# Performance work log

Measured on AMD Instinct MI355X. Metric: run time of the kernel, lower is better.

Reference implementation:

```python
import jax, jax.numpy as jnp
import numpy as np

B, N, H = 8, 2000, 64  # batch, num_nodes(=input_dim), hidden(num_gru_units)


def _laplacian_self_loop(a):
    # batched: norm = D^{-1/2} (A + I) D^{-1/2}
    m = a + jnp.eye(a.shape[-1], dtype=a.dtype)
    d_inv_sqrt = jnp.sum(m, axis=-1) ** -0.5  # (B, N)
    return d_inv_sqrt[..., :, None] * m * d_inv_sqrt[..., None, :]


def _graph_conv(inputs, hidden_flat, adj, windd, W2, b2, W3, b3, W, b, out_dim):
    b_, _, n = inputs.shape
    # dynamic wind-based adjacency
    wind_now = inputs[:, 2, :] * 360.0  # (B, N)
    direction = jnp.abs(windd[None, :, :] - wind_now[:, :, None])  # (B, N, N)
    direction = jnp.where(direction > 360.0, 180.0, direction)
    d1 = jnp.maximum(jnp.cos(direction * (jnp.pi / 180.0)), 0.0)
    a = d1 @ W2.T + b2 + (adj @ W3.T + b3)[None]  # (B, N, N)
    a1 = _laplacian_self_loop(jnp.maximum(a, 0.0))
    # graph conv: concat [x, h] then A @ [.] then Linear
    x = jnp.concatenate([inputs[:, 0, :, None], hidden_flat.reshape(b_, n, H)], axis=2)  # (B,N,H+1)
    y = jnp.einsum('bij,bjh->bih', a1, x) @ W.T + b  # (B, N, out_dim)
    return y.reshape(b_, n * out_dim)


def reference(inputs, hidden_state, adj, windd, W2, b2, W3, b3, W1a, b1a, W1b, b1b, Wca1, Wca2, Wsa):
    b_, _, n = inputs.shape
    conc = _graph_conv(inputs, hidden_state, adj, windd, W2, b2, W3, b3, W1a, b1a, 2 * H)
    conc = conc.reshape(b_, 2 * H, n)  # faithful reshape (input_dim == N)
    # --- channel attention (CBAM) ---
    avg = jnp.mean(conc, axis=2, keepdims=True)  # (B, 2H, 1)
    mx = jnp.max(conc, axis=2, keepdims=True)
    def fc(v):
        return jnp.einsum('oc,bcx->box', Wca2, jax.nn.relu(jnp.einsum('oc,bcx->box', Wca1, v)))
    ca = jax.nn.sigmoid(fc(avg) + fc(mx))  # (B, 2H, 1)
    conc = ca * conc
    # --- spatial attention ---
    s = jnp.stack([jnp.mean(conc, axis=1), jnp.max(conc, axis=1)], axis=1)  # (B, 2, N)
    sa = jax.lax.conv_general_dilated(s, Wsa, window_strides=(1,), padding=((3, 3),),
                                      dimension_numbers=('NCH', 'OIH', 'NCH'))  # (B,1,N)
    conc = jax.nn.sigmoid(sa) * conc
    # --- GRU gates ---
    conc = jax.nn.sigmoid(conc.reshape(b_, 2 * H * n))
    r, u = jnp.split(conc, 2, axis=1)  # each (B, N*H)
    c = jnp.tanh(_graph_conv(inputs, r * hidden_state, adj, windd, W2, b2, W3, b3, W1b, b1b, H))
    new_hidden_state = u * hidden_state + (1.0 - u) * c
    return new_hidden_state


def setup_inputs() -> dict:
    key = jax.random.key(0)
    ks = jax.random.split(key, 12)
    inputs = jax.random.uniform(ks[0], (B, 3, N), dtype=jnp.float32)
    hidden_state = jax.random.normal(ks[1], (B, N * H), dtype=jnp.float32) * 0.1
    adj = jax.random.uniform(ks[2], (N, N), dtype=jnp.float32)
    windd = jax.random.uniform(ks[3], (N, N), dtype=jnp.float32) * 360.0
    sN = 1.0 / np.sqrt(N)
    W2 = jax.random.normal(ks[4], (N, N), dtype=jnp.float32) * sN
    b2 = jnp.zeros((N,), jnp.float32)
    W3 = jax.random.normal(ks[5], (N, N), dtype=jnp.float32) * sN
    b3 = jnp.zeros((N,), jnp.float32)
    sI = 1.0 / np.sqrt(H + 1)
    W1a = jax.random.normal(ks[6], (2 * H, H + 1), dtype=jnp.float32) * sI
    b1a = jnp.ones((2 * H,), jnp.float32)  # bias=1.0 in graph_conv1
    W1b = jax.random.normal(ks[7], (H, H + 1), dtype=jnp.float32) * sI
    b1b = jnp.zeros((H,), jnp.float32)
    Wca1 = jax.random.normal(ks[8], (2 * H // 16, 2 * H), dtype=jnp.float32) * (1.0 / np.sqrt(2 * H))
    Wca2 = jax.random.normal(ks[9], (2 * H, 2 * H // 16), dtype=jnp.float32) * (1.0 / np.sqrt(2 * H // 16))
    Wsa = jax.random.normal(ks[10], (1, 2, 7), dtype=jnp.float32) * (1.0 / np.sqrt(14))
    return {'inputs': inputs, 'hidden_state': hidden_state, 'adj': adj, 'windd': windd,
            'W2': W2, 'b2': b2, 'W3': W3, 'b3': b3, 'W1a': W1a, 'b1a': b1a,
            'W1b': W1b, 'b1b': b1b, 'Wca1': Wca1, 'Wca2': Wca2, 'Wsa': Wsa}
```

## Files before the change

### kernel.cpp

```cpp
#include <hip/hip_runtime.h>

#define NN 2000
#define BB 8
#define P  2048

typedef __attribute__((ext_vector_type(8))) short bf16x8;
typedef __attribute__((ext_vector_type(4))) float f32x4;

__device__ __forceinline__ float sigf(float x) { return 1.0f / (1.0f + expf(-x)); }

__device__ __forceinline__ short f2bf(float x) {
    union { float f; unsigned u; } v; v.f = x;
    unsigned r = v.u + 0x7fffu + ((v.u >> 16) & 1u);
    return (short)(r >> 16);
}
__device__ __forceinline__ float bf2f(short h) {
    union { unsigned u; float f; } v; v.u = ((unsigned)(unsigned short)h) << 16; return v.f;
}

__device__ __forceinline__ void gl2lds16(const short* g, short* l) {
    __builtin_amdgcn_global_load_lds(
        (const __attribute__((address_space(1))) void*)g,
        (__attribute__((address_space(3))) void*)l, 16, 0, 0);
}

__global__ __launch_bounds__(256) void k_cvtW(
    const float* __restrict__ s0, const float* __restrict__ s1, const float* __restrict__ s2,
    short* __restrict__ d0, short* __restrict__ d1, short* __restrict__ d2)
{
    const int i = blockIdx.x, sel = blockIdx.y, t = threadIdx.x;
    const float* s = (sel == 0) ? s0 : (sel == 1) ? s1 : s2;
    short* d = ((sel == 0) ? d0 : (sel == 1) ? d1 : d2) + ((size_t)i) * P + t * 8;
    bf16x8 v;
#pragma unroll
    for (int e = 0; e < 8; ++e) v[e] = 0;
    if (i < NN && t < 250) {
        const float* p = s + (size_t)i * NN + t * 8;
        float4 x0 = *(const float4*)p;
        float4 x1 = *(const float4*)(p + 4);
        float a[8] = {x0.x,x0.y,x0.z,x0.w,x1.x,x1.y,x1.z,x1.w};
#pragma unroll
        for (int e = 0; e < 8; ++e) v[e] = f2bf(a[e]);
    }
    *(bf16x8*)d = v;
}

__global__ __launch_bounds__(256) void k_cvtD1(
    const float* __restrict__ windd, const float* __restrict__ inputs, short* __restrict__ d1bf)
{
    const int i = blockIdx.x, t = threadIdx.x;
    const bool live = (i < NN) && (t < 250);
    float a[8];
    if (live) {
        const float* p = windd + (size_t)i * NN + t * 8;
        float4 x0 = *(const float4*)p;
        float4 x1 = *(const float4*)(p + 4);
        a[0]=x0.x; a[1]=x0.y; a[2]=x0.z; a[3]=x0.w;
        a[4]=x1.x; a[5]=x1.y; a[6]=x1.z; a[7]=x1.w;
    }
#pragma unroll
    for (int b = 0; b < BB; ++b) {
        bf16x8 v;
#pragma unroll
        for (int e = 0; e < 8; ++e) v[e] = 0;
        if (live) {
            const float wn = inputs[(size_t)b * 3 * NN + 2 * NN + i] * 360.0f;
#pragma unroll
            for (int e = 0; e < 8; ++e) {
                float dd = fabsf(a[e] - wn);
                dd = (dd > 360.0f) ? 180.0f : dd;
                float c = __cosf(dd * 0.01745329251994329577f);
                v[e] = f2bf(fmaxf(c, 0.0f));
            }
        }
        *(bf16x8*)(d1bf + ((size_t)b * P + i) * P + t * 8) = v;
    }
}

template<int EPI, int OUTD>
__global__ __launch_bounds__(256) void k_mfma(
    const short* __restrict__ Abase, const short* __restrict__ Bbase,
    const float* __restrict__ bias, const short* __restrict__ adjw,
    void* __restrict__ Cout, float* __restrict__ part, size_t aBatch)
{
    __shared__ short shA[4096];
    __shared__ short shB[4096];
    const int t = threadIdx.x;
    const int w = t >> 6, lane = t & 63;
    const int wr = w >> 1, wc = w & 1;

    int i0, j0, b, kt = 0;
    if (EPI == 1) {
        const int id = blockIdx.x;
        const int lg = (id & 7) * 256 + (id >> 3);
        b = lg >> 8;
        const int rem = lg & 255;
        i0 = (rem >> 4) * 128;
        j0 = (rem & 15) * 128;
    } else if (EPI == 2) {
        i0 = blockIdx.x * 128; j0 = 0; kt = blockIdx.y; b = blockIdx.z;
    } else {
        i0 = blockIdx.x * 128; j0 = blockIdx.y * 128; b = 0;
    }
    const int kb = (EPI == 2) ? kt * (P / 4) : 0;
    const int ke = (EPI == 2) ? kt * (P / 4) + (P / 4) : P;

    const short* A  = Abase + (size_t)b * aBatch;
    const short* Bm = Bbase + ((EPI == 2) ? (size_t)b * 128 * P : (size_t)0);

    f32x4 acc[4][4];
#pragma unroll
    for (int m = 0; m < 4; ++m)
#pragma unroll
        for (int n = 0; n < 4; ++n) acc[m][n] = (f32x4){0.f, 0.f, 0.f, 0.f};

    const int lidx0 = w * 128 + lane;
    const int lidx1 = lidx0 + 64;
    const short* aS0 = A  + (size_t)(i0 + (lidx0 >> 2)) * P + (lidx0 & 3) * 8;
    const short* aS1 = A  + (size_t)(i0 + (lidx1 >> 2)) * P + (lidx1 & 3) * 8;
    const short* bS0 = Bm + (size_t)(j0 + (lidx0 >> 2)) * P + (lidx0 & 3) * 8;
    const short* bS1 = Bm + (size_t)(j0 + (lidx1 >> 2)) * P + (lidx1 & 3) * 8;
    short* ldA0 = shA + (w * 128) * 8;
    short* ldA1 = shA + (w * 128 + 64) * 8;
    short* ldB0 = shB + (w * 128) * 8;
    short* ldB1 = shB + (w * 128 + 64) * 8;

    const int lr = lane & 15, lq = lane >> 4;
    const int aoff = (wr * 64 + lr) * 32 + lq * 8;
    const int boff = (wc * 64 + lr) * 32 + lq * 8;

    for (int k0 = kb; k0 < ke; k0 += 32) {
        gl2lds16(aS0 + k0, ldA0);
        gl2lds16(aS1 + k0, ldA1);
        gl2lds16(bS0 + k0, ldB0);
        gl2lds16(bS1 + k0, ldB1);
        __syncthreads();
        bf16x8 aF[4], bF[4];
#pragma unroll
        for (int m = 0; m < 4; ++m) aF[m] = *(const bf16x8*)(shA + aoff + m * 512);
#pragma unroll
        for (int n = 0; n < 4; ++n) bF[n] = *(const bf16x8*)(shB + boff + n * 512);
#pragma unroll
        for (int m = 0; m < 4; ++m)
#pragma unroll
            for (int n = 0; n < 4; ++n)
                acc[m][n] = __builtin_amdgcn_mfma_f32_16x16x32_bf16(aF[m], bF[n], acc[m][n], 0, 0, 0);
        __syncthreads();
    }

    const int rbase = i0 + wr * 64 + lq * 4;
    const int cbase = j0 + wc * 64 + lr;
#pragma unroll
    for (int m = 0; m < 4; ++m) {
#pragma unroll
        for (int n = 0; n < 4; ++n) {
            const int col = cbase + n * 16;
#pragma unroll
            for (int q = 0; q < 4; ++q) {
                const int row = rbase + m * 16 + q;
                float v = acc[m][n][q];
                if (EPI == 0) {
                    if (row < NN && col < NN)
                        ((short*)Cout)[(size_t)row * NN + col] = f2bf(v + bias[col]);
                } else if (EPI == 1) {
                    short o = 0;
                    if (row < NN && col < NN) {
                        float x = v + bias[col] + bf2f(adjw[(size_t)row * NN + col]);
                        x = fmaxf(x, 0.0f);
                        if (row == col) x += 1.0f;
                        o = f2bf(x);
                    }
                    ((short*)Cout)[((size_t)b * P + row) * P + col] = o;
                } else {
                    if (row < NN && col < OUTD)
                        part[((size_t)(kt * BB + b) * NN + row) * OUTD + col] = v;
                }
            }
        }
    }
}

template<int OUTD>
__global__ __launch_bounds__(256) void k_comb(
    const float* __restrict__ part, const float* __restrict__ dinv,
    const float* __restrict__ bias, float* __restrict__ out)
{
    const size_t idx = (size_t)blockIdx.x * 256 + threadIdx.x;
    const size_t S = (size_t)BB * NN * OUTD;
    if (idx >= S) return;
    const int o = (int)(idx % OUTD);
    const size_t r = idx / OUTD;
    const int i = (int)(r % NN);
    const int b = (int)(r / NN);
    float s = ((part[idx] + part[idx + S]) + (part[idx + 2 * S] + part[idx + 3 * S]));
    out[idx] = s * dinv[b * NN + i] + bias[o];
}

__global__ __launch_bounds__(256) void k_rowsum_bf(const short* __restrict__ m_bf, float* __restrict__ dinv)
{
    const int i = blockIdx.x, b = blockIdx.y;
    const short* p = m_bf + ((size_t)b * P + i) * P + threadIdx.x * 8;
    bf16x8 v = *(const bf16x8*)p;
    float s = 0.0f;
#pragma unroll
    for (int e = 0; e < 8; ++e) s += bf2f(v[e]);
#pragma unroll
    for (int off = 32; off > 0; off >>= 1) s += __shfl_down(s, off);
    __shared__ float red[4];
    if ((threadIdx.x & 63) == 0) red[threadIdx.x >> 6] = s;
    __syncthreads();
    if (threadIdx.x == 0) dinv[b * NN + i] = rsqrtf(red[0] + red[1] + red[2] + red[3]);
}

template<int OUT>
__global__ __launch_bounds__(128) void k_xwT(
    const float* __restrict__ inputs, const float* __restrict__ hsrc,
    const float* __restrict__ W, const float* __restrict__ dinv, short* __restrict__ zT)
{
    const int b = blockIdx.y;
    const int j0 = blockIdx.x * 16;
    const int t = threadIdx.x;
    __shared__ float wl[128 * 65];
    __shared__ float xs[16 * 66];
    __shared__ float dj[16];
    for (int idx = t; idx < OUT * 65; idx += 128) wl[idx] = W[idx];
    for (int idx = t; idx < 16 * 64; idx += 128) {
        int jj = idx >> 6, hh = idx & 63, j = j0 + jj;
        xs[jj * 66 + 1 + hh] = (j < NN) ? hsrc[((size_t)b * NN + j) * 64 + hh] : 0.0f;
    }
    if (t < 16) {
        int j = j0 + t;
        xs[t * 66] = (j < NN) ? inputs[(size_t)b * 3 * NN + j] : 0.0f;
        dj[t] = (j < NN) ? dinv[b * NN + j] : 0.0f;
    }
    __syncthreads();
    for (int jj = 0; jj < 16; ++jj) {
        float a = 0.0f;
        if (t < OUT) {
            const float* xr = &xs[jj * 66];
            const float* wr = &wl[t * 65];
#pragma unroll
            for (int c = 0; c < 65; ++c) a = fmaf(xr[c], wr[c], a);
        }
        int j = j0 + jj;
        zT[((size_t)b * 128 + t) * P + j] = (t < OUT && j < NN) ? f2bf(a * dj[jj]) : (short)0;
    }
}

__global__ __launch_bounds__(256) void k_chred(const float* __restrict__ conc,
                                               float* __restrict__ avg, float* __restrict__ mx)
{
    const int bc = blockIdx.x;
    const float* p = conc + (size_t)bc * NN;
    float s = 0.0f, mv = -3.402823466e+38f;
    for (int n = threadIdx.x; n < NN; n += 256) { float v = p[n]; s += v; mv = fmaxf(mv, v); }
#pragma unroll
    for (int off = 32; off > 0; off >>= 1) {
        s += __shfl_down(s, off);
        mv = fmaxf(mv, __shfl_down(mv, off));
    }
    __shared__ float rs[4], rm[4];
    if ((threadIdx.x & 63) == 0) { rs[threadIdx.x >> 6] = s; rm[threadIdx.x >> 6] = mv; }
    __syncthreads();
    if (threadIdx.x == 0) {
        avg[bc] = (rs[0] + rs[1] + rs[2] + rs[3]) * (1.0f / NN);
        mx[bc]  = fmaxf(fmaxf(rm[0], rm[1]), fmaxf(rm[2], rm[3]));
    }
}

__global__ __launch_bounds__(128) void k_ca(
    const float* __restrict__ avg, const float* __restrict__ mx,
    const float* __restrict__ Wca1, const float* __restrict__ Wca2, float* __restrict__ ca)
{
    const int b = blockIdx.x, t = threadIdx.x;
    __shared__ float av[128], mv[128], h[16];
    av[t] = avg[b * 128 + t];
    mv[t] = mx[b * 128 + t];
    __syncthreads();
    if (t < 16) {
        int o8 = t & 7;
        const float* src = (t < 8) ? av : mv;
        float s = 0.0f;
        for (int c = 0; c < 128; ++c) s = fmaf(Wca1[o8 * 128 + c], src[c], s);
        h[t] = fmaxf(s, 0.0f);
    }
    __syncthreads();
    float s = 0.0f;
#pragma unroll
    for (int k = 0; k < 8; ++k) s = fmaf(Wca2[t * 8 + k], h[k] + h[8 + k], s);
    ca[b * 128 + t] = sigf(s);
}

__global__ __launch_bounds__(256) void k_sat(
    const float* __restrict__ conc, const float* __restrict__ ca,
    float* __restrict__ s0, float* __restrict__ s1)
{
    const int b = blockIdx.y;
    const int n = blockIdx.x * 256 + threadIdx.x;
    __shared__ float cas[128];
    if (threadIdx.x < 128) cas[threadIdx.x] = ca[b * 128 + threadIdx.x];
    __syncthreads();
    if (n >= NN) return;
    float sm = 0.0f, sx = -3.402823466e+38f;
    for (int c = 0; c < 128; ++c) {
        float v = cas[c] * conc[(size_t)b * NN * 128 + (size_t)c * NN + n];
        sm += v; sx = fmaxf(sx, v);
    }
    s0[b * NN + n] = sm * (1.0f / 128.0f);
    s1[b * NN + n] = sx;
}

__global__ __launch_bounds__(256) void k_gate(
    const float* __restrict__ conc, const float* __restrict__ ca,
    const float* __restrict__ s0, const float* __restrict__ s1,
    const float* __restrict__ Wsa, const float* __restrict__ hidden,
    float* __restrict__ rh, float* __restrict__ u)
{
    const int b = blockIdx.y;
    const int n = blockIdx.x * 256 + threadIdx.x;
    __shared__ float cas[128];
    __shared__ float wsa[14];
    if (threadIdx.x < 128) cas[threadIdx.x] = ca[b * 128 + threadIdx.x];
    if (threadIdx.x < 14) wsa[threadIdx.x] = Wsa[threadIdx.x];
    __syncthreads();
    if (n >= NN) return;
    float sa = 0.0f;
#pragma unroll
    for (int k = 0; k < 7; ++k) {
        int nn = n + k - 3;
        if (nn >= 0 && nn < NN)
            sa += wsa[k] * s0[b * NN + nn] + wsa[7 + k] * s1[b * NN + nn];
    }
    float gs = sigf(sa);
    for (int c = 0; c < 128; ++c) {
        float v = gs * cas[c] * conc[(size_t)b * NN * 128 + (size_t)c * NN + n];
        float g = sigf(v);
        if (c < 64)
            rh[(size_t)b * NN * 64 + (size_t)c * NN + n] =
                g * hidden[(size_t)b * NN * 64 + (size_t)c * NN + n];
        else
            u[(size_t)b * NN * 64 + (size_t)(c - 64) * NN + n] = g;
    }
}

__global__ __launch_bounds__(256) void k_fin(
    const float* __restrict__ u, const float* __restrict__ hidden,
    const float* __restrict__ cpre, float* __restrict__ out)
{
    const size_t idx = (size_t)blockIdx.x * 256 + threadIdx.x;
    if (idx >= (size_t)BB * NN * 64) return;
    float uu = u[idx];
    out[idx] = uu * hidden[idx] + (1.0f - uu) * tanhf(cpre[idx]);
}

extern "C" void kernel_launch(void* const* d_in, const int* in_sizes, int n_in,
                              void* d_out, int out_size, void* d_ws, size_t ws_size,
                              hipStream_t stream)
{
    (void)in_sizes; (void)n_in; (void)out_size; (void)ws_size;
    const float* inputs = (const float*)d_in[0];
    const float* hidden = (const float*)d_in[1];
    const float* adj    = (const float*)d_in[2];
    const float* windd  = (const float*)d_in[3];
    const float* W2     = (const float*)d_in[4];
    const float* b2     = (const float*)d_in[5];
    const float* W3     = (const float*)d_in[6];
    const float* b3     = (const float*)d_in[7];
    const float* W1a    = (const float*)d_in[8];
    const float* b1a    = (const float*)d_in[9];
    const float* W1b    = (const float*)d_in[10];
    const float* b1b    = (const float*)d_in[11];
    const float* Wca1   = (const float*)d_in[12];
    const float* Wca2   = (const float*)d_in[13];
    const float* Wsa    = (const float*)d_in[14];
    float* out = (float*)d_out;

    char* W = (char*)d_ws;
    short* adjW3bf = (short*)(W + 0);
    short* W2bf    = (short*)(W + 8000000);
    short* W3bf    = (short*)(W + 16388608);
    short* adjbf   = (short*)(W + 24777216);
    short* m_bf    = (short*)(W + 16388608);
    char* D = W + 83497472;
    short* d1bf = (short*)D;
    float* dinv = (float*)(D + 0);
    float* avgb = (float*)(D + 64000);
    float* mxb  = (float*)(D + 68096);
    float* cab  = (float*)(D + 72192);
    float* s0b  = (float*)(D + 76288);
    float* s1b  = (float*)(D + 140288);
    short* zT   = (short*)(D + 204800);
    float* conc = (float*)(D + 4399104);
    float* rh   = (float*)(D + 12591104);
    float* ubuf = (float*)(D + 16687104);
    float* cpre = (float*)(D + 20783104);
    float* part = (float*)(D + 24879104);

    const size_t PP = (size_t)P * P;

    k_cvtW<<<dim3(P, 3), 256, 0, stream>>>(W2, W3, adj, W2bf, W3bf, adjbf);
    k_cvtD1<<<P, 256, 0, stream>>>(windd, inputs, d1bf);
    k_mfma<0, 0><<<dim3(16, 16, 1), 256, 0, stream>>>(adjbf, W3bf, b3, nullptr, adjW3bf, nullptr, 0);
    k_mfma<1, 0><<<2048, 256, 0, stream>>>(d1bf, W2bf, b2, adjW3bf, m_bf, nullptr, PP);
    k_rowsum_bf<<<dim3(NN, BB), 256, 0, stream>>>(m_bf, dinv);
    k_xwT<128><<<dim3(128, BB), 128, 0, stream>>>(inputs, hidden, W1a, dinv, zT);
    k_mfma<2, 128><<<dim3(16, 4, BB), 256, 0, stream>>>(m_bf, zT, nullptr, nullptr, nullptr, part, PP);
    k_comb<128><<<(BB * NN * 128 + 255) / 256, 256, 0, stream>>>(part, dinv, b1a, conc);
    k_chred<<<BB * 128, 256, 0, stream>>>(conc, avgb, mxb);
    k_ca<<<BB, 128, 0, stream>>>(avgb, mxb, Wca1, Wca2, cab);
    k_sat<<<dim3(8, BB), 256, 0, stream>>>(conc, cab, s0b, s1b);
    k_gate<<<dim3(8, BB), 256, 0, stream>>>(conc, cab, s0b, s1b, Wsa, hidden, rh, ubuf);
    k_xwT<64><<<dim3(128, BB), 128, 0, stream>>>(inputs, rh, W1b, dinv, zT);
    k_mfma<2, 64><<<dim3(16, 4, BB), 256, 0, stream>>>(m_bf, zT, nullptr, nullptr, nullptr, part, PP);
    k_comb<64><<<(BB * NN * 64 + 255) / 256, 256, 0, stream>>>(part, dinv, b1b, cpre);
    k_fin<<<(BB * NN * 64 + 255) / 256, 256, 0, stream>>>(ubuf, hidden, cpre, out);
}
```

Before: 455.9 us.

## Replace batched d1@W2 GEMM with 256x256-tile 8-wave pipelined MFMA kernel

Swaps the 128x128-tile, 4-wave GEMM that builds the batched dynamic adjacency for a dedicated kernel using 256x256 tiles and 8 waves. It double-buffers LDS (128KB) with direct global-to-LDS loads, an XOR swizzle, and four phases per k-step that interleave loads with MFMA under setprio and explicit waitcnt/barrier control. The goal is higher arithmetic intensity and better overlap of memory with MFMA on the dominant 8x2048^3 GEMM. In exchange, the large LDS and register footprint may limit occupancy, and the hand-tuned synchronization is fragile.

```diff
diff --git a/kernel.cpp b/kernel.cpp
--- a/kernel.cpp
+++ b/kernel.cpp
@@ -3,6 +3,7 @@
 #define NN 2000
 #define BB 8
 #define P  2048
+#define NT 32
 
 typedef __attribute__((ext_vector_type(8))) short bf16x8;
 typedef __attribute__((ext_vector_type(4))) float f32x4;
@@ -77,6 +78,183 @@
     }
 }
 
+__global__ __launch_bounds__(512, 2) void k_g8p(
+    const short* __restrict__ d1bf, const short* __restrict__ W2bf,
+    const float* __restrict__ b2, const short* __restrict__ adjw,
+    short* __restrict__ m_bf)
+{
+    __shared__ char smem[131072];
+    const int t = threadIdx.x;
+    const int w = t >> 6, lane = t & 63;
+    const int wm = w >> 2, wn = w & 3;
+    const int lr = lane & 15, lq = lane >> 4;
+    const int tile = blockIdx.x;
+    const int b = blockIdx.y;
+    const int i0 = (tile >> 3) * 256, j0 = (tile & 7) * 256;
+    const short* A  = d1bf + (size_t)b * P * P;
+    const short* Bm = W2bf;
+
+    const int e0 = w * 64 + lane;
+    const int e1 = 512 + e0;
+    const int r0 = e0 >> 3, r1 = e1 >> 3;
+    const int lc0 = (e0 & 7) ^ (r0 & 7);
+    const int lc1 = (e1 & 7) ^ (r1 & 7);
+    const short* s0q0 = A + (size_t)(i0 + r0) * P + lc0 * 8;
+    const short* s0q1 = A + (size_t)(i0 + r1 + 64) * P + lc1 * 8;
+    const short* s2q0 = A + (size_t)(i0 + r0 + 64) * P + lc0 * 8;
+    const short* s2q1 = A + (size_t)(i0 + r1 + 128) * P + lc1 * 8;
+    const int c0 = (r0 >> 5) * 64 + (r0 & 31);
+    const int c1 = (r1 >> 5) * 64 + (r1 & 31);
+    const short* s1q0 = Bm + (size_t)(j0 + c0) * P + lc0 * 8;
+    const short* s1q1 = Bm + (size_t)(j0 + c1) * P + lc1 * 8;
+    const short* s3q0 = Bm + (size_t)(j0 + c0 + 32) * P + lc0 * 8;
+    const short* s3q1 = Bm + (size_t)(j0 + c1 + 32) * P + lc1 * 8;
+    const int aB0 = w * 1024;
+    const int aB1 = 16384 + w * 1024;
+    const int bB0 = (w >> 2) * 8192 + (w & 3) * 1024;
+    const int bB1 = 16384 + (w >> 2) * 8192 + (w & 3) * 1024;
+
+    const int fx0 = (lq * 16) ^ ((lr & 7) << 4);
+    const int fx1 = ((4 + lq) * 16) ^ ((lr & 7) << 4);
+    const int arow = (wm * 128 + lr) * 128;
+    const int brow = (wn * 64 + lr) * 128;
+
+    f32x4 acc[8][4];
+#pragma unroll
+    for (int m = 0; m < 8; ++m)
+#pragma unroll
+        for (int n = 0; n < 4; ++n) acc[m][n] = (f32x4){0.f, 0.f, 0.f, 0.f};
+    bf16x8 aF[4][2], bF0[2][2], bF1[2][2];
+
+    gl2lds16(s0q0, (short*)(smem + aB0));
+    gl2lds16(s0q1, (short*)(smem + aB1));
+    gl2lds16(s1q0, (short*)(smem + 65536 + bB0));
+    gl2lds16(s1q1, (short*)(smem + 65536 + bB1));
+    gl2lds16(s3q0, (short*)(smem + 65536 + 4096 + bB0));
+    gl2lds16(s3q1, (short*)(smem + 65536 + 4096 + bB1));
+    gl2lds16(s2q0, (short*)(smem + 8192 + aB0));
+    gl2lds16(s2q1, (short*)(smem + 8192 + aB1));
+    asm volatile("s_waitcnt vmcnt(0)" ::: "memory");
+    __builtin_amdgcn_s_barrier();
+    asm volatile("" ::: "memory");
+
+#define MFMA_(a, bq, m, n) acc[m][n] = __builtin_amdgcn_mfma_f32_16x16x32_bf16(a, bq, acc[m][n], 0, 0, 0)
+#define PHASE_TAIL()                                     \
+    __builtin_amdgcn_s_setprio(0);                       \
+    __builtin_amdgcn_sched_barrier(0);                   \
+    asm volatile("s_waitcnt vmcnt(4)" ::: "memory");     \
+    __builtin_amdgcn_s_barrier();                        \
+    asm volatile("" ::: "memory")
+#define PHASE_MID()                                      \
+    __builtin_amdgcn_s_barrier();                        \
+    asm volatile("s_waitcnt lgkmcnt(0)" ::: "memory");   \
+    __builtin_amdgcn_sched_barrier(0);                   \
+    __builtin_amdgcn_s_setprio(1)
+
+    for (int kt = 0; kt < NT; ++kt) {
+        char* curA = smem + (kt & 1) * 32768;
+        char* curB = smem + 65536 + (kt & 1) * 32768;
+        char* stgA = smem + ((kt + 1) & 1) * 32768;
+        char* stgB = smem + 65536 + ((kt + 1) & 1) * 32768;
+        const int ktn = (kt + 1 < NT) ? (kt + 1) : (NT - 1);
+        const size_t kO = (size_t)ktn * 64;
+
+#pragma unroll
+        for (int m = 0; m < 4; ++m) {
+            aF[m][0] = *(const bf16x8*)(curA + arow + m * 2048 + fx0);
+            aF[m][1] = *(const bf16x8*)(curA + arow + m * 2048 + fx1);
+        }
+#pragma unroll
+        for (int n = 0; n < 2; ++n) {
+            bF0[n][0] = *(const bf16x8*)(curB + brow + n * 2048 + fx0);
+            bF0[n][1] = *(const bf16x8*)(curB + brow + n * 2048 + fx1);
+        }
+        gl2lds16(s0q0 + kO, (short*)(stgA + aB0));
+        gl2lds16(s0q1 + kO, (short*)(stgA + aB1));
+        PHASE_MID();
+#pragma unroll
+        for (int m = 0; m < 4; ++m)
+#pragma unroll
+            for (int n = 0; n < 2; ++n) {
+                MFMA_(aF[m][0], bF0[n][0], m, n);
+                MFMA_(aF[m][1], bF0[n][1], m, n);
+            }
+        PHASE_TAIL();
+
+#pragma unroll
+        for (int n = 0; n < 2; ++n) {
+            bF1[n][0] = *(const bf16x8*)(curB + brow + (n + 2) * 2048 + fx0);
+            bF1[n][1] = *(const bf16x8*)(curB + brow + (n + 2) * 2048 + fx1);
+        }
+        gl2lds16(s1q0 + kO, (short*)(stgB + bB0));
+        gl2lds16(s1q1 + kO, (short*)(stgB + bB1));
+        PHASE_MID();
+#pragma unroll
+        for (int m = 0; m < 4; ++m)
+#pragma unroll
+            for (int n = 0; n < 2; ++n) {
+                MFMA_(aF[m][0], bF1[n][0], m, n + 2);
+                MFMA_(aF[m][1], bF1[n][1], m, n + 2);
+            }
+        PHASE_TAIL();
+
+#pragma unroll
+        for (int m = 0; m < 4; ++m) {
+            aF[m][0] = *(const bf16x8*)(curA + arow + (m + 4) * 2048 + fx0);
+            aF[m][1] = *(const bf16x8*)(curA + arow + (m + 4) * 2048 + fx1);
+        }
+        gl2lds16(s3q0 + kO, (short*)(stgB + 4096 + bB0));
+        gl2lds16(s3q1 + kO, (short*)(stgB + 4096 + bB1));
+        PHASE_MID();
+#pragma unroll
+        for (int m = 0; m < 4; ++m)
+#pragma unroll
+            for (int n = 0; n < 2; ++n) {
+                MFMA_(aF[m][0], bF0[n][0], m + 4, n);
+                MFMA_(aF[m][1], bF0[n][1], m + 4, n);
+            }
+        PHASE_TAIL();
+
+        gl2lds16(s2q0 + kO, (short*)(stgA + 8192 + aB0));
+        gl2lds16(s2q1 + kO, (short*)(stgA + 8192 + aB1));
+        PHASE_MID();
+#pragma unroll
+        for (int m = 0; m < 4; ++m)
+#pragma unroll
+            for (int n = 0; n < 2; ++n) {
+                MFMA_(aF[m][0], bF1[n][0], m + 4, n + 2);
+                MFMA_(aF[m][1], bF1[n][1], m + 4, n + 2);
+            }
+        PHASE_TAIL();
+    }
+    asm volatile("s_waitcnt vmcnt(0)" ::: "memory");
+
+    const int rbase = i0 + wm * 128 + lq * 4;
+    const int cbase = j0 + wn * 64 + lr;
+#pragma unroll
+    for (int m = 0; m < 8; ++m) {
+#pragma unroll
+        for (int n = 0; n < 4; ++n) {
+            const int col = cbase + n * 16;
+#pragma unroll
+            for (int q = 0; q < 4; ++q) {
+                const int row = rbase + m * 16 + q;
+                short o = 0;
+                if (row < NN && col < NN) {
+                    float x = acc[m][n][q] + b2[col] + bf2f(adjw[(size_t)row * NN + col]);
+                    x = fmaxf(x, 0.0f);
+                    if (row == col) x += 1.0f;
+                    o = f2bf(x);
+                }
+                m_bf[((size_t)b * P + row) * P + col] = o;
+            }
+        }
+    }
+#undef MFMA_
+#undef PHASE_TAIL
+#undef PHASE_MID
+}
+
 template<int EPI, int OUTD>
 __global__ __launch_bounds__(256) void k_mfma(
     const short* __restrict__ Abase, const short* __restrict__ Bbase,
@@ -90,14 +268,7 @@
     const int wr = w >> 1, wc = w & 1;
 
     int i0, j0, b, kt = 0;
-    if (EPI == 1) {
-        const int id = blockIdx.x;
-        const int lg = (id & 7) * 256 + (id >> 3);
-        b = lg >> 8;
-        const int rem = lg & 255;
-        i0 = (rem >> 4) * 128;
-        j0 = (rem & 15) * 128;
-    } else if (EPI == 2) {
+    if (EPI == 2) {
         i0 = blockIdx.x * 128; j0 = 0; kt = blockIdx.y; b = blockIdx.z;
     } else {
         i0 = blockIdx.x * 128; j0 = blockIdx.y * 128; b = 0;
@@ -162,15 +333,6 @@
                 if (EPI == 0) {
                     if (row < NN && col < NN)
                         ((short*)Cout)[(size_t)row * NN + col] = f2bf(v + bias[col]);
-                } else if (EPI == 1) {
-                    short o = 0;
-                    if (row < NN && col < NN) {
-                        float x = v + bias[col] + bf2f(adjw[(size_t)row * NN + col]);
-                        x = fmaxf(x, 0.0f);
-                        if (row == col) x += 1.0f;
-                        o = f2bf(x);
-                    }
-                    ((short*)Cout)[((size_t)b * P + row) * P + col] = o;
                 } else {
                     if (row < NN && col < OUTD)
                         part[((size_t)(kt * BB + b) * NN + row) * OUTD + col] = v;
@@ -401,7 +563,7 @@
     k_cvtW<<<dim3(P, 3), 256, 0, stream>>>(W2, W3, adj, W2bf, W3bf, adjbf);
     k_cvtD1<<<P, 256, 0, stream>>>(windd, inputs, d1bf);
     k_mfma<0, 0><<<dim3(16, 16, 1), 256, 0, stream>>>(adjbf, W3bf, b3, nullptr, adjW3bf, nullptr, 0);
-    k_mfma<1, 0><<<2048, 256, 0, stream>>>(d1bf, W2bf, b2, adjW3bf, m_bf, nullptr, PP);
+    k_g8p<<<dim3(64, BB), 512, 0, stream>>>(d1bf, W2bf, b2, adjW3bf, m_bf);
     k_rowsum_bf<<<dim3(NN, BB), 256, 0, stream>>>(m_bf, dinv);
     k_xwT<128><<<dim3(128, BB), 128, 0, stream>>>(inputs, hidden, W1a, dinv, zT);
     k_mfma<2, 128><<<dim3(16, 4, BB), 256, 0, stream>>>(m_bf, zT, nullptr, nullptr, nullptr, part, PP);
```

After: 430.4 us. 1.06x faster.

## Replace batched d1·W2ᵀ GEMM with 256x256-tile 4-stage pipelined MFMA kernel; fuse spatial-attention kernels

Applied to the files above, without the earlier changes.

The dominant batched GEMM (d1 @ W2ᵀ with the ReLU/adjacency epilogue) moves to a new 512-thread kernel. It uses 256x256 output tiles, a 4-slot LDS ring filled by direct global-to-LDS loads, XOR-swizzled addressing, and explicit barrier, waitcnt and setprio scheduling so loads overlap with MFMA work. The larger tiles are meant to cut global traffic per FLOP and to hide memory latency. The trade-off is 128KB of LDS, a 64x8 grid of only 512 blocks, and heavy register use from the 8x4 accumulators. Separately, the spatial-attention reduction and gate kernels are merged, recomputing halo columns, which drops one launch and the s0/s1 round trip.

```diff
diff --git a/kernel.cpp b/kernel.cpp
--- a/kernel.cpp
+++ b/kernel.cpp
@@ -3,6 +3,7 @@
 #define NN 2000
 #define BB 8
 #define P  2048
+#define NKT 64
 
 typedef __attribute__((ext_vector_type(8))) short bf16x8;
 typedef __attribute__((ext_vector_type(4))) float f32x4;
@@ -77,6 +78,126 @@
     }
 }
 
+__global__ __launch_bounds__(512, 2) void k_g4s(
+    const short* __restrict__ d1bf, const short* __restrict__ W2bf,
+    const float* __restrict__ b2, const short* __restrict__ adjw,
+    short* __restrict__ m_bf)
+{
+    __shared__ char smem[131072];
+    const int t = threadIdx.x;
+    const int w = t >> 6, lane = t & 63;
+    const int wm = w >> 2, wn = w & 3;
+    const int lr = lane & 15, lq = lane >> 4;
+    const int tile = blockIdx.x;
+    const int b = blockIdx.y;
+    const int i0 = (tile & 7) * 256;
+    const int j0 = (tile >> 3) * 256;
+    const short* A  = d1bf + (size_t)b * P * P;
+    const short* Bm = W2bf;
+
+    const int cA0 = w * 64 + lane, cA1 = cA0 + 512;
+    const int rA0 = cA0 >> 2, rA1 = cA1 >> 2;
+    const short* srcA0 = A + (size_t)(i0 + rA0) * P + (((cA0 & 3) ^ ((rA0 >> 2) & 3)) * 8);
+    const short* srcA1 = A + (size_t)(i0 + rA1) * P + (((cA1 & 3) ^ ((rA1 >> 2) & 3)) * 8);
+    const short* srcB0 = Bm + (size_t)(j0 + rA0) * P + (((cA0 & 3) ^ ((rA0 >> 2) & 3)) * 8);
+    const short* srcB1 = Bm + (size_t)(j0 + rA1) * P + (((cA1 & 3) ^ ((rA1 >> 2) & 3)) * 8);
+
+#define STAGE_A(slot, ktI) do {                                                   \
+        gl2lds16(srcA0 + (ktI) * 32, (short*)(smem + (slot) * 16384 + w * 1024)); \
+        gl2lds16(srcA1 + (ktI) * 32, (short*)(smem + (slot) * 16384 + 8192 + w * 1024)); } while (0)
+#define STAGE_B(slot, ktI) do {                                                   \
+        gl2lds16(srcB0 + (ktI) * 32, (short*)(smem + 65536 + (slot) * 16384 + w * 1024)); \
+        gl2lds16(srcB1 + (ktI) * 32, (short*)(smem + 65536 + (slot) * 16384 + 8192 + w * 1024)); } while (0)
+
+    const int fch = (lq ^ (lr >> 2)) << 4;
+    const int arowB = (wm * 128 + lr) * 64 + fch;
+    const int browB = (wn * 64 + lr) * 64 + fch;
+
+    f32x4 acc[8][4];
+#pragma unroll
+    for (int m = 0; m < 8; ++m)
+#pragma unroll
+        for (int n = 0; n < 4; ++n) acc[m][n] = (f32x4){0.f, 0.f, 0.f, 0.f};
+    bf16x8 aF[4], bF[4];
+
+    STAGE_A(0, 0); STAGE_B(0, 0);
+    STAGE_A(1, 1); STAGE_B(1, 1);
+    STAGE_A(2, 2); STAGE_B(2, 2);
+    asm volatile("s_waitcnt vmcnt(0)" ::: "memory");
+    __builtin_amdgcn_s_barrier();
+    asm volatile("" ::: "memory");
+
+#define MFMA_(a_, b_, m, n) acc[m][n] = __builtin_amdgcn_mfma_f32_16x16x32_bf16(a_, b_, acc[m][n], 0, 0, 0)
+#define PHASE_MID()                                      \
+    __builtin_amdgcn_s_barrier();                        \
+    asm volatile("s_waitcnt lgkmcnt(0)" ::: "memory");   \
+    __builtin_amdgcn_sched_barrier(0);                   \
+    __builtin_amdgcn_s_setprio(1)
+#define PHASE_TAIL()                                     \
+    __builtin_amdgcn_s_setprio(0);                       \
+    __builtin_amdgcn_sched_barrier(0);                   \
+    asm volatile("s_waitcnt vmcnt(8)" ::: "memory");     \
+    __builtin_amdgcn_s_barrier();                        \
+    asm volatile("" ::: "memory")
+
+    for (int kt = 0; kt < NKT; ++kt) {
+        char* curA = smem + (kt & 3) * 16384;
+        char* curB = smem + 65536 + (kt & 3) * 16384;
+        const int stgSlot = (kt + 3) & 3;
+        const int stgKt = (kt + 3 < NKT) ? (kt + 3) : (NKT - 1);
+
+#pragma unroll
+        for (int m = 0; m < 4; ++m) aF[m] = *(const bf16x8*)(curA + arowB + m * 1024);
+#pragma unroll
+        for (int n = 0; n < 4; ++n) bF[n] = *(const bf16x8*)(curB + browB + n * 1024);
+        STAGE_A(stgSlot, stgKt);
+        PHASE_MID();
+#pragma unroll
+        for (int m = 0; m < 4; ++m)
+#pragma unroll
+            for (int n = 0; n < 4; ++n) MFMA_(aF[m], bF[n], m, n);
+        PHASE_TAIL();
+
+#pragma unroll
+        for (int m = 0; m < 4; ++m) aF[m] = *(const bf16x8*)(curA + arowB + (m + 4) * 1024);
+        STAGE_B(stgSlot, stgKt);
+        PHASE_MID();
+#pragma unroll
+        for (int m = 0; m < 4; ++m)
+#pragma unroll
+            for (int n = 0; n < 4; ++n) MFMA_(aF[m], bF[n], m + 4, n);
+        PHASE_TAIL();
+    }
+    asm volatile("s_waitcnt vmcnt(0)" ::: "memory");
+
+    const int rbase = i0 + wm * 128 + lq * 4;
+    const int cbase = j0 + wn * 64 + lr;
+#pragma unroll
+    for (int m = 0; m < 8; ++m) {
+#pragma unroll
+        for (int n = 0; n < 4; ++n) {
+            const int col = cbase + n * 16;
+#pragma unroll
+            for (int q = 0; q < 4; ++q) {
+                const int row = rbase + m * 16 + q;
+                short o = 0;
+                if (row < NN && col < NN) {
+                    float x = acc[m][n][q] + b2[col] + bf2f(adjw[(size_t)row * NN + col]);
+                    x = fmaxf(x, 0.0f);
+                    if (row == col) x += 1.0f;
+                    o = f2bf(x);
+                }
+                m_bf[((size_t)b * P + row) * P + col] = o;
+            }
+        }
+    }
+#undef MFMA_
+#undef PHASE_MID
+#undef PHASE_TAIL
+#undef STAGE_A
+#undef STAGE_B
+}
+
 template<int EPI, int OUTD>
 __global__ __launch_bounds__(256) void k_mfma(
     const short* __restrict__ Abase, const short* __restrict__ Bbase,
@@ -90,14 +211,7 @@
     const int wr = w >> 1, wc = w & 1;
 
     int i0, j0, b, kt = 0;
-    if (EPI == 1) {
-        const int id = blockIdx.x;
-        const int lg = (id & 7) * 256 + (id >> 3);
-        b = lg >> 8;
-        const int rem = lg & 255;
-        i0 = (rem >> 4) * 128;
-        j0 = (rem & 15) * 128;
-    } else if (EPI == 2) {
+    if (EPI == 2) {
         i0 = blockIdx.x * 128; j0 = 0; kt = blockIdx.y; b = blockIdx.z;
     } else {
         i0 = blockIdx.x * 128; j0 = blockIdx.y * 128; b = 0;
@@ -162,15 +276,6 @@
                 if (EPI == 0) {
                     if (row < NN && col < NN)
                         ((short*)Cout)[(size_t)row * NN + col] = f2bf(v + bias[col]);
-                } else if (EPI == 1) {
-                    short o = 0;
-                    if (row < NN && col < NN) {
-                        float x = v + bias[col] + bf2f(adjw[(size_t)row * NN + col]);
-                        x = fmaxf(x, 0.0f);
-                        if (row == col) x += 1.0f;
-                        o = f2bf(x);
-                    }
-                    ((short*)Cout)[((size_t)b * P + row) * P + col] = o;
                 } else {
                     if (row < NN && col < OUTD)
                         part[((size_t)(kt * BB + b) * NN + row) * OUTD + col] = v;
@@ -291,49 +396,58 @@
     ca[b * 128 + t] = sigf(s);
 }
 
-__global__ __launch_bounds__(256) void k_sat(
+__global__ __launch_bounds__(256) void k_satgate(
     const float* __restrict__ conc, const float* __restrict__ ca,
-    float* __restrict__ s0, float* __restrict__ s1)
-{
-    const int b = blockIdx.y;
-    const int n = blockIdx.x * 256 + threadIdx.x;
-    __shared__ float cas[128];
-    if (threadIdx.x < 128) cas[threadIdx.x] = ca[b * 128 + threadIdx.x];
-    __syncthreads();
-    if (n >= NN) return;
-    float sm = 0.0f, sx = -3.402823466e+38f;
-    for (int c = 0; c < 128; ++c) {
-        float v = cas[c] * conc[(size_t)b * NN * 128 + (size_t)c * NN + n];
-        sm += v; sx = fmaxf(sx, v);
-    }
-    s0[b * NN + n] = sm * (1.0f / 128.0f);
-    s1[b * NN + n] = sx;
-}
-
-__global__ __launch_bounds__(256) void k_gate(
-    const float* __restrict__ conc, const float* __restrict__ ca,
-    const float* __restrict__ s0, const float* __restrict__ s1,
     const float* __restrict__ Wsa, const float* __restrict__ hidden,
     float* __restrict__ rh, float* __restrict__ u)
 {
     const int b = blockIdx.y;
-    const int n = blockIdx.x * 256 + threadIdx.x;
+    const int n0 = blockIdx.x * 256;
+    const int t = threadIdx.x;
     __shared__ float cas[128];
     __shared__ float wsa[14];
-    if (threadIdx.x < 128) cas[threadIdx.x] = ca[b * 128 + threadIdx.x];
-    if (threadIdx.x < 14) wsa[threadIdx.x] = Wsa[threadIdx.x];
-    __syncthreads();
+    __shared__ float s0l[262], s1l[262];
+    if (t < 128) cas[t] = ca[b * 128 + t];
+    if (t >= 128 && t < 142) wsa[t - 128] = Wsa[t - 128];
+    __syncthreads();
+
+    const float* cb = conc + (size_t)b * NN * 128;
+    {
+        const int n = n0 + t;
+        float sm = 0.0f, sx = -3.402823466e+38f;
+        if (n < NN) {
+            for (int c = 0; c < 128; ++c) {
+                float v = cas[c] * cb[(size_t)c * NN + n];
+                sm += v; sx = fmaxf(sx, v);
+            }
+            s0l[t + 3] = sm * (1.0f / 128.0f);
+            s1l[t + 3] = sx;
+        } else { s0l[t + 3] = 0.0f; s1l[t + 3] = 0.0f; }
+    }
+    if (t < 6) {
+        const int hn = (t < 3) ? (n0 - 3 + t) : (n0 + 256 + (t - 3));
+        const int hi = (t < 3) ? t : (256 + t);
+        float sm = 0.0f, sx = -3.402823466e+38f;
+        if (hn >= 0 && hn < NN) {
+            for (int c = 0; c < 128; ++c) {
+                float v = cas[c] * cb[(size_t)c * NN + hn];
+                sm += v; sx = fmaxf(sx, v);
+            }
+            s0l[hi] = sm * (1.0f / 128.0f);
+            s1l[hi] = sx;
+        } else { s0l[hi] = 0.0f; s1l[hi] = 0.0f; }
+    }
+    __syncthreads();
+
+    const int n = n0 + t;
     if (n >= NN) return;
     float sa = 0.0f;
 #pragma unroll
-    for (int k = 0; k < 7; ++k) {
-        int nn = n + k - 3;
-        if (nn >= 0 && nn < NN)
-            sa += wsa[k] * s0[b * NN + nn] + wsa[7 + k] * s1[b * NN + nn];
-    }
+    for (int k = 0; k < 7; ++k)
+        sa += wsa[k] * s0l[t + k] + wsa[7 + k] * s1l[t + k];
     float gs = sigf(sa);
     for (int c = 0; c < 128; ++c) {
-        float v = gs * cas[c] * conc[(size_t)b * NN * 128 + (size_t)c * NN + n];
+        float v = gs * cas[c] * cb[(size_t)c * NN + n];
         float g = sigf(v);
         if (c < 64)
             rh[(size_t)b * NN * 64 + (size_t)c * NN + n] =
@@ -387,8 +501,6 @@
     float* avgb = (float*)(D + 64000);
     float* mxb  = (float*)(D + 68096);
     float* cab  = (float*)(D + 72192);
-    float* s0b  = (float*)(D + 76288);
-    float* s1b  = (float*)(D + 140288);
     short* zT   = (short*)(D + 204800);
     float* conc = (float*)(D + 4399104);
     float* rh   = (float*)(D + 12591104);
@@ -401,15 +513,14 @@
     k_cvtW<<<dim3(P, 3), 256, 0, stream>>>(W2, W3, adj, W2bf, W3bf, adjbf);
     k_cvtD1<<<P, 256, 0, stream>>>(windd, inputs, d1bf);
     k_mfma<0, 0><<<dim3(16, 16, 1), 256, 0, stream>>>(adjbf, W3bf, b3, nullptr, adjW3bf, nullptr, 0);
-    k_mfma<1, 0><<<2048, 256, 0, stream>>>(d1bf, W2bf, b2, adjW3bf, m_bf, nullptr, PP);
+    k_g4s<<<dim3(64, BB), 512, 0, stream>>>(d1bf, W2bf, b2, adjW3bf, m_bf);
     k_rowsum_bf<<<dim3(NN, BB), 256, 0, stream>>>(m_bf, dinv);
     k_xwT<128><<<dim3(128, BB), 128, 0, stream>>>(inputs, hidden, W1a, dinv, zT);
     k_mfma<2, 128><<<dim3(16, 4, BB), 256, 0, stream>>>(m_bf, zT, nullptr, nullptr, nullptr, part, PP);
     k_comb<128><<<(BB * NN * 128 + 255) / 256, 256, 0, stream>>>(part, dinv, b1a, conc);
     k_chred<<<BB * 128, 256, 0, stream>>>(conc, avgb, mxb);
     k_ca<<<BB, 128, 0, stream>>>(avgb, mxb, Wca1, Wca2, cab);
-    k_sat<<<dim3(8, BB), 256, 0, stream>>>(conc, cab, s0b, s1b);
-    k_gate<<<dim3(8, BB), 256, 0, stream>>>(conc, cab, s0b, s1b, Wsa, hidden, rh, ubuf);
+    k_satgate<<<dim3(8, BB), 256, 0, stream>>>(conc, cab, Wsa, hidden, rh, ubuf);
     k_xwT<64><<<dim3(128, BB), 128, 0, stream>>>(inputs, rh, W1b, dinv, zT);
     k_mfma<2, 64><<<dim3(16, 4, BB), 256, 0, stream>>>(m_bf, zT, nullptr, nullptr, nullptr, part, PP);
     k_comb<64><<<(BB * NN * 64 + 255) / 256, 256, 0, stream>>>(part, dinv, b1b, cpre);
```

Measured after the change: 442.4 us. -3.0%, faster.
